# Kernel optimization log

Hardware: AMD Instinct MI355X
Metric: run time of the kernel (lower is better)

The kernel has to match this reference:

```python
import jax, jax.numpy as jnp
import numpy as np
from jax import lax

NUM_HEADS = 8

def _conv2d(x, w, b, padding, rhs_dilation=(1, 1)):
    # x: NCHW, w: OIHW
    out = lax.conv_general_dilated(x, w, (1, 1), padding,
                                   rhs_dilation=rhs_dilation,
                                   dimension_numbers=('NCHW', 'OIHW', 'NCHW'))
    return out + b[None, :, None, None]

def _bn(x, scale, bias):
    # eval-mode batchnorm folded into per-channel affine
    return x * scale[None, :, None, None] + bias[None, :, None, None]

def setup_inputs() -> dict:
    key = jax.random.key(0)
    ks = jax.random.split(key, 12)
    B, C, H, W = 16, 256, 64, 64
    D = C // 2          # down_dim = 128
    Dq = D // 16        # weight bottleneck = 8
    return {
        'x':          jax.random.normal(ks[0], (B, C, H, W), jnp.float32),
        'conv2_w':    jax.random.normal(ks[1], (D, C, 3, 3), jnp.float32) * 0.02,
        'conv2_b':    jnp.zeros((D,), jnp.float32),
        'bn2_scale':  jax.random.uniform(ks[2], (D,), jnp.float32, 0.5, 1.5),
        'bn2_bias':   jax.random.normal(ks[3], (D,), jnp.float32) * 0.1,
        'temperature': jnp.ones((NUM_HEADS, 1, 1), jnp.float32),
        'w1_w':       jax.random.normal(ks[4], (Dq, D, 1, 1), jnp.float32) * 0.05,
        'w1_b':       jnp.zeros((Dq,), jnp.float32),
        'bnw_scale':  jax.random.uniform(ks[5], (Dq,), jnp.float32, 0.5, 1.5),
        'bnw_bias':   jax.random.normal(ks[6], (Dq,), jnp.float32) * 0.1,
        'w2_w':       jax.random.normal(ks[7], (D, Dq, 1, 1), jnp.float32) * 0.05,
        'w2_b':       jnp.zeros((D,), jnp.float32),
    }

def _l2_normalize_complex(z, eps=1e-12):
    # torch F.normalize on complex: divide by L2 norm of |z| along last dim
    n = jnp.sqrt(jnp.sum(jnp.real(z * jnp.conj(z)), axis=-1, keepdims=True))
    return z / jnp.maximum(n, eps)

def reference(x, conv2_w, conv2_b, bn2_scale, bn2_bias, temperature,
              w1_w, w1_b, bnw_scale, bnw_bias, w2_w, w2_b):
    # conv2 branch: 3x3 conv with dilation=3, padding=3 -> BN -> ReLU
    conv2 = jax.nn.relu(_bn(_conv2d(x, conv2_w, conv2_b,
                                    ((3, 3), (3, 3)), rhs_dilation=(3, 3)),
                            bn2_scale, bn2_bias))
    b, c, h, w = conv2.shape
    f = jnp.fft.fft2(conv2)                      # complex64, (b,c,h,w); q=k=v=tepqkv
    cp = c // NUM_HEADS
    qkv = f.reshape(b, NUM_HEADS, cp, h * w)     # 'b (head c) h w -> b head c (h w)'
    qn = _l2_normalize_complex(qkv)
    kn = qn
    # complex attention logits, temperature broadcast over heads
    attn = jnp.einsum('bhin,bhjn->bhij', qn, kn) * temperature.astype(attn_dtype := qn.dtype)
    # dual real/imag softmax reassembled into complex
    attn = lax.complex(jax.nn.softmax(attn.real, axis=-1),
                       jax.nn.softmax(attn.imag, axis=-1))
    out_f = jnp.einsum('bhij,bhjn->bhin', attn, qkv)
    # torch.fft.ifft2 default dims=(-2,-1): here over (c, h*w) axes — faithful
    out_f = jnp.abs(jnp.fft.ifft2(out_f)).reshape(b, c, h, w)
    # gating branch on real part of spectrum
    g = jax.nn.relu(_bn(_conv2d(f.real, w1_w, w1_b, ((0, 0), (0, 0))),
                        bnw_scale, bnw_bias))
    g = jax.nn.sigmoid(_conv2d(g, w2_w, w2_b, ((0, 0), (0, 0))))
    out_l = jnp.abs(jnp.fft.ifft2(g * f))        # ifft2 over (h, w)
    out = jnp.concatenate([out_f, out_l], axis=1)
    return out + x
```

## Files before the change

kernel.cpp:

```cpp
#include <hip/hip_runtime.h>

typedef unsigned short u16;
typedef short short8 __attribute__((ext_vector_type(8)));
typedef float f32x4 __attribute__((ext_vector_type(4)));

#define MF(a,b,c) __builtin_amdgcn_mfma_f32_16x16x32_bf16(a,b,c,0,0,0)

__device__ __forceinline__ float bu2f(u16 u){
  return __uint_as_float(((unsigned int)u) << 16);
}
__device__ __forceinline__ u16 f2bu(float f){
  unsigned int b = __float_as_uint(f);
  unsigned int r = (b + 0x7FFFu + ((b >> 16) & 1u)) >> 16;
  return (u16)r;
}
__device__ __forceinline__ void ld4a(float* d, const float* p){
  float4 v = *(const float4*)p;
  d[0]=v.x; d[1]=v.y; d[2]=v.z; d[3]=v.w;
}
__device__ __forceinline__ void st4(float* p, const float* s){
  *(float4*)p = make_float4(s[0], s[1], s[2], s[3]);
}
__device__ __forceinline__ void ld4b(float* d, const u16* p){
  ushort4 v = *(const ushort4*)p;
  d[0]=bu2f(v.x); d[1]=bu2f(v.y); d[2]=bu2f(v.z); d[3]=bu2f(v.w);
}
__device__ __forceinline__ void st4b(u16* p, const float* s){
  ushort4 v;
  v.x=f2bu(s[0]); v.y=f2bu(s[1]); v.z=f2bu(s[2]); v.w=f2bu(s[3]);
  *(ushort4*)p = v;
}
__device__ __forceinline__ ushort4 pk4(f32x4 v){
  ushort4 u; u.x=f2bu(v[0]); u.y=f2bu(v[1]); u.z=f2bu(v[2]); u.w=f2bu(v[3]); return u;
}
__device__ __forceinline__ short8 mulpk(short8 g, short8 f){
  short8 o;
  #pragma unroll
  for (int e = 0; e < 8; ++e)
    o[e] = (short)f2bu(bu2f((u16)g[e])*bu2f((u16)f[e]));
  return o;
}

#define TABF_RE   0
#define TABF_IM   4096
#define TABIF_RE  8192
#define TABIF_IM  12288
#define TABTW_RE  16384
#define TABTW_IM  20480
#define NORMS_OFF 24576
#define MMAT_OFF  26624
#define FLAG_OFF  92160
#define PRM_OFF   92224
#define WT_OFF    94848
#define DFT16_OFF 242304
#define F32_END   389760
#define P_CB   0
#define P_BNS  128
#define P_BNB  256
#define P_TEMP 384
#define P_W1   400
#define P_B1   1424
#define P_S1   1432
#define P_BB1  1440
#define P_W2   1456
#define P_B2   2480
#define BPLANE    8388608

__global__ void k_detect(const u16* __restrict__ xv, int* __restrict__ flag){
  const int t = threadIdx.x;
  int huge = 0;
  for (int i = 0; i < 16; ++i){
    u16 u = xv[(t*16 + i)*2];
    int e = (u >> 7) & 0xFF;
    huge += (e >= 0xC0) ? 1 : 0;
  }
  #pragma unroll
  for (int off = 32; off > 0; off >>= 1) huge += __shfl_down(huge, off, 64);
  if (t == 0) flag[0] = (huge >= 8) ? 1 : 0;
}

__global__ void k_tables(float* ws){
  int idx = blockIdx.x*256 + threadIdx.x;
  int j = idx >> 6, k = idx & 63;
  int jk = j*k;
  float s, c;
  sincospif(-(float)(jk & 63)/32.0f, &s, &c);
  ws[TABF_RE+idx] = c; ws[TABF_IM+idx] = s;
  sincospif((float)(jk & 63)/32.0f, &s, &c);
  ws[TABIF_RE+idx] = c*(1.f/64.f); ws[TABIF_IM+idx] = s*(1.f/64.f);
  sincospif((float)jk/2048.0f, &s, &c);
  ws[TABTW_RE+idx] = c; ws[TABTW_IM+idx] = s;
}

__global__ void k_dftprep(u16* __restrict__ m){
  int idx = blockIdx.x*256 + threadIdx.x;
  int j = idx >> 6, k = idx & 63;
  int jk = (j*k) & 63;
  float s, c;
  sincospif(-(float)jk/32.0f, &s, &c);
  m[idx]        = f2bu(c);
  m[4096+idx]   = f2bu(s);
  sincospif((float)jk/32.0f, &s, &c);
  m[8192+idx]   = f2bu(c*(1.f/64.f));
  m[12288+idx]  = f2bu(s*(1.f/64.f));
}

__global__ void k_pack(const void* cb, const void* bns, const void* bnb, const void* temp,
                       const void* w1, const void* b1, const void* s1, const void* bb1,
                       const void* w2, const void* b2,
                       const int* __restrict__ flg, float* __restrict__ P){
  const int t = threadIdx.x;
  const int f32 = *flg;
  if (f32){
    for (int i = t; i < 128; i += 256){
      P[P_CB+i]  = ((const float*)cb)[i];
      P[P_BNS+i] = ((const float*)bns)[i];
      P[P_BNB+i] = ((const float*)bnb)[i];
      P[P_B2+i]  = ((const float*)b2)[i];
    }
    for (int i = t; i < 1024; i += 256){
      P[P_W1+i] = ((const float*)w1)[i];
      P[P_W2+i] = ((const float*)w2)[i];
    }
    if (t < 8){
      P[P_TEMP+t] = ((const float*)temp)[t];
      P[P_B1+t]   = ((const float*)b1)[t];
      P[P_S1+t]   = ((const float*)s1)[t];
      P[P_BB1+t]  = ((const float*)bb1)[t];
    }
  } else {
    for (int i = t; i < 128; i += 256){
      P[P_CB+i]  = bu2f(((const u16*)cb)[i]);
      P[P_BNS+i] = bu2f(((const u16*)bns)[i]);
      P[P_BNB+i] = bu2f(((const u16*)bnb)[i]);
      P[P_B2+i]  = bu2f(((const u16*)b2)[i]);
    }
    for (int i = t; i < 1024; i += 256){
      P[P_W1+i] = bu2f(((const u16*)w1)[i]);
      P[P_W2+i] = bu2f(((const u16*)w2)[i]);
    }
    if (t < 8){
      P[P_TEMP+t] = bu2f(((const u16*)temp)[t]);
      P[P_B1+t]   = bu2f(((const u16*)b1)[t]);
      P[P_S1+t]   = bu2f(((const u16*)s1)[t]);
      P[P_BB1+t]  = bu2f(((const u16*)bb1)[t]);
    }
  }
}

__global__ void k_wprep2(const void* __restrict__ w, u16* __restrict__ wT2,
                         const float* __restrict__ prm, const int* __restrict__ flg){
  const int f32 = *flg;
  int U = blockIdx.x*256 + threadIdx.x;
  if (U < 294912){
    int j = U & 7;
    int E = U >> 3;
    int n = E & 127;
    int o = (E >> 7) & 3;
    int tc = E >> 9;
    int chunk = tc & 7, tap = tc >> 3;
    int c = chunk*32 + o*8 + j;
    int src = n*2304 + c*9 + tap;
    float v = f32 ? ((const float*)w)[src] : bu2f(((const u16*)w)[src]);
    wT2[U] = f2bu(v * prm[P_BNS + n]);
  }
}

__global__ __launch_bounds__(256) void k_trans(const void* __restrict__ x, u16* __restrict__ xt,
                                               const int* __restrict__ flg){
  __shared__ u16 L[256*66];
  const int t = threadIdx.x;
  const int b = blockIdx.x >> 6, h = blockIdx.x & 63;
  const int f32m = __builtin_amdgcn_readfirstlane(*flg);
  if (f32m){
    const float* xf = (const float*)x;
    for (int i = t; i < 16384; i += 256){
      int c = i >> 6, w = i & 63;
      L[c*66 + w] = f2bu(xf[((b*256 + c)*64 + h)*64 + w]);
    }
  } else {
    const u16* xb = (const u16*)x;
    for (int i = t; i < 16384; i += 256){
      int c = i >> 6, w = i & 63;
      L[c*66 + w] = xb[((b*256 + c)*64 + h)*64 + w];
    }
  }
  __syncthreads();
  u16* dst = xt + ((b*64 + h)*64)*256;
  for (int j = t; j < 16384; j += 256){
    int w = j >> 8, c = j & 255;
    dst[w*256 + c] = L[c*66 + w];
  }
}

__global__ __launch_bounds__(512) void k_cmm(const u16* __restrict__ xt, const u16* __restrict__ wT2,
                                             const float* __restrict__ prm, u16* __restrict__ A){
  __shared__ __align__(16) uint4 smW4[8192];
  const int t = threadIdx.x;
  const int bb = blockIdx.x >> 4;
  const int mtile = blockIdx.x & 15;
  const int h0 = mtile*4;
  const int lane = t & 63, wave = t >> 6;
  const int wrow = wave >> 1, wcol = wave & 1;
  const int quad = lane >> 4, lr = lane & 15;

  f32x4 acc[4][4];
  #pragma unroll
  for (int mi = 0; mi < 4; ++mi)
    #pragma unroll
    for (int j = 0; j < 4; ++j)
      acc[mi][j] = (f32x4){0.f,0.f,0.f,0.f};

  const short8 zz = {0,0,0,0,0,0,0,0};

  {
    const uint4* src = (const uint4*)wT2;
    uint4 stg[8];
    #pragma unroll
    for (int i = 0; i < 8; ++i) stg[i] = src[t + 512*i];
    #pragma unroll
    for (int i = 0; i < 8; ++i) smW4[t + 512*i] = stg[i];
  }
  __syncthreads();

  for (int tap = 0; tap < 9; ++tap){
    const int buf = tap & 1;
    const int ky = tap/3, kx = tap - ky*3;

    uint4 stg[8];
    if (tap < 8){
      const uint4* src = (const uint4*)(wT2 + (tap+1)*32768);
      #pragma unroll
      for (int i = 0; i < 8; ++i) stg[i] = src[t + 512*i];
    }

    const u16* smB = (const u16*)(smW4 + buf*4096);
    const int hg = h0 + wrow + 3*ky - 3;
    const bool hok = ((unsigned)hg < 64u);
    const u16* abase = xt + ((bb*64 + hg)*64)*256 + quad*8;

    for (int chunk = 0; chunk < 8; ++chunk){
      short8 av[4];
      #pragma unroll
      for (int mi = 0; mi < 4; ++mi){
        const int wg = mi*16 + lr + 3*kx - 3;
        short8 v = zz;
        if (hok && ((unsigned)wg < 64u))
          v = *(const short8*)(abase + wg*256 + chunk*32);
        av[mi] = v;
      }
      short8 bv[4];
      #pragma unroll
      for (int j = 0; j < 4; ++j)
        bv[j] = *(const short8*)(smB + (chunk*512 + quad*128 + (wcol*4+j)*16 + lr)*8);
      #pragma unroll
      for (int mi = 0; mi < 4; ++mi)
        #pragma unroll
        for (int j = 0; j < 4; ++j)
          acc[mi][j] = MF(av[mi], bv[j], acc[mi][j]);
    }

    if (tap < 8){
      uint4* dst = smW4 + (buf^1)*4096;
      #pragma unroll
      for (int i = 0; i < 8; ++i) dst[t + 512*i] = stg[i];
    }
    __syncthreads();
  }

  float* C = (float*)smW4;
  u16* outb = A + (bb*128)*4096 + mtile*256;
  const int ch32 = wcol*16 + lr;
  for (int nt2 = 0; nt2 < 4; ++nt2){
    #pragma unroll
    for (int mi = 0; mi < 4; ++mi)
      #pragma unroll
      for (int r = 0; r < 4; ++r){
        const int m = wrow*64 + mi*16 + quad*4 + r;
        C[ch32*261 + m] = acc[mi][nt2][r];
      }
    __syncthreads();
    #pragma unroll
    for (int dd = 0; dd < 16; ++dd){
      const int idx = dd*512 + t;
      const int c32 = idx >> 8, m = idx & 255;
      const int d = (c32 >> 4)*64 + nt2*16 + (c32 & 15);
      const float bi = prm[P_CB + d]*prm[P_BNS + d] + prm[P_BNB + d];
      const float v = fmaxf(C[c32*261 + m] + bi, 0.f);
      outb[d*4096 + m] = f2bu(v);
    }
    __syncthreads();
  }
}

__global__ __launch_bounds__(256) void k_fft2_m(const u16* __restrict__ A, u16* __restrict__ Frb,
                                                u16* __restrict__ Fib, const u16* __restrict__ dft){
  __shared__ __align__(16) u16 TTr[64*72], TTi[64*72];
  const int bc = blockIdx.x, t = threadIdx.x;
  const int lane = t & 63, wave = t >> 6;
  const int quad = lane >> 4, lr = lane & 15;
  const u16* EFr = dft;
  const u16* EFi = dft + 4096;
  const u16* img = A + bc*4096;
  #pragma unroll
  for (int mi = 0; mi < 4; ++mi){
    f32x4 ar = {0.f,0.f,0.f,0.f}, ai = {0.f,0.f,0.f,0.f};
    #pragma unroll
    for (int ks = 0; ks < 2; ++ks){
      short8 av = *(const short8*)(img + (mi*16+lr)*64 + ks*32 + quad*8);
      short8 br = *(const short8*)(EFr + (wave*16+lr)*64 + ks*32 + quad*8);
      short8 bi = *(const short8*)(EFi + (wave*16+lr)*64 + ks*32 + quad*8);
      ar = MF(av, br, ar); ai = MF(av, bi, ai);
    }
    *(ushort4*)(TTr + (wave*16+lr)*72 + mi*16 + quad*4) = pk4(ar);
    *(ushort4*)(TTi + (wave*16+lr)*72 + mi*16 + quad*4) = pk4(ai);
  }
  __syncthreads();
  #pragma unroll
  for (int nt = 0; nt < 4; ++nt){
    f32x4 a1={0.f,0.f,0.f,0.f}, a2={0.f,0.f,0.f,0.f}, a3={0.f,0.f,0.f,0.f}, a4={0.f,0.f,0.f,0.f};
    #pragma unroll
    for (int ks = 0; ks < 2; ++ks){
      short8 tr = *(const short8*)(TTr + (wave*16+lr)*72 + ks*32 + quad*8);
      short8 ti = *(const short8*)(TTi + (wave*16+lr)*72 + ks*32 + quad*8);
      short8 br = *(const short8*)(EFr + (nt*16+lr)*64 + ks*32 + quad*8);
      short8 bi = *(const short8*)(EFi + (nt*16+lr)*64 + ks*32 + quad*8);
      a1 = MF(tr, br, a1); a2 = MF(ti, bi, a2);
      a3 = MF(tr, bi, a3); a4 = MF(ti, br, a4);
    }
    f32x4 fr, fi;
    #pragma unroll
    for (int r = 0; r < 4; ++r){ fr[r] = a1[r]-a2[r]; fi[r] = a3[r]+a4[r]; }
    const int flat = (nt*16+lr)*64 + wave*16 + quad*4;
    *(ushort4*)(Frb + bc*4096 + flat) = pk4(fr);
    *(ushort4*)(Fib + bc*4096 + flat) = pk4(fi);
  }
}

__global__ __launch_bounds__(256) void k_attn1(const u16* __restrict__ Frb,
                                               const u16* __restrict__ Fib,
                                               float* __restrict__ part){
  __shared__ float R[4][4][256];
  const int blk = blockIdx.x;
  const int bh = blk >> 4, chunk = blk & 15;
  const int t = threadIdx.x, lane = t & 63, wave = t >> 6;
  const int quad = lane >> 4, lr = lane & 15;
  const u16* fr = Frb + bh*65536;
  const u16* fi = Fib + bh*65536;
  const int c0 = chunk*256 + wave*64;
  f32x4 a1={0.f,0.f,0.f,0.f}, a2={0.f,0.f,0.f,0.f}, a3={0.f,0.f,0.f,0.f}, a4={0.f,0.f,0.f,0.f};
  #pragma unroll
  for (int ks = 0; ks < 2; ++ks){
    const int off = lr*4096 + c0 + ks*32 + quad*8;
    short8 ar = *(const short8*)(fr + off);
    short8 ai = *(const short8*)(fi + off);
    a1 = MF(ar, ar, a1); a2 = MF(ai, ai, a2);
    a3 = MF(ar, ai, a3); a4 = MF(ai, ar, a4);
  }
  #pragma unroll
  for (int r = 0; r < 4; ++r){
    const int mn = (quad*4 + r)*16 + lr;
    R[wave][0][mn] = a1[r];
    R[wave][1][mn] = a2[r];
    R[wave][2][mn] = a3[r];
    R[wave][3][mn] = a4[r];
  }
  __syncthreads();
  float* dst = part + blk*1024;
  #pragma unroll
  for (int q = 0; q < 4; ++q)
    dst[q*256 + t] = R[0][q][t] + R[1][q][t] + R[2][q][t] + R[3][q][t];
}

__global__ __launch_bounds__(256) void k_attn2(const float* __restrict__ part,
                                               const float* __restrict__ prm,
                                               float* __restrict__ wsM){
  __shared__ float AR[16][17], AI[16][17], NR[16];
  const int bh = blockIdx.x;
  const int h = bh & 7;
  const int t = threadIdx.x;
  const float* p = part + bh*16384;
  float s1=0.f, s2=0.f, s3=0.f, s4=0.f;
  #pragma unroll
  for (int ch = 0; ch < 16; ++ch){
    s1 += p[ch*1024 +       t];
    s2 += p[ch*1024 + 256 + t];
    s3 += p[ch*1024 + 512 + t];
    s4 += p[ch*1024 + 768 + t];
  }
  const int m = t >> 4, n = t & 15;
  if (m == n) NR[m] = fmaxf(sqrtf(fmaxf(s1 + s2, 0.f)), 1e-12f);
  __syncthreads();
  const float sc = prm[P_TEMP + h] / (NR[m]*NR[n]);
  AR[m][n] = (s1 - s2)*sc;
  AI[m][n] = (s3 + s4)*sc;
  __syncthreads();
  if (t < 32){
    float* row = (t < 16) ? AR[t & 15] : AI[t & 15];
    float mx = row[0];
    for (int j2 = 1; j2 < 16; ++j2) mx = fmaxf(mx, row[j2]);
    float s = 0.f, e[16];
    for (int j2 = 0; j2 < 16; ++j2){ e[j2] = expf(row[j2] - mx); s += e[j2]; }
    float inv = 1.f/s;
    for (int j2 = 0; j2 < 16; ++j2) row[j2] = e[j2]*inv;
  }
  __syncthreads();
  {
    const int mi = t >> 4, mj = t & 15;
    float mr = 0.f, mim = 0.f;
    #pragma unroll
    for (int pp = 0; pp < 16; ++pp){
      float sv, cv;
      sincospif((float)((mi*pp) & 15)/8.0f, &sv, &cv);
      const float arv = AR[pp][mj], aiv = AI[pp][mj];
      mr  += cv*arv - sv*aiv;
      mim += cv*aiv + sv*arv;
    }
    wsM[bh*512 + t*2]     = mr*(1.f/16.f);
    wsM[bh*512 + t*2 + 1] = mim*(1.f/16.f);
  }
}

__global__ __launch_bounds__(256) void k_gate(const u16* __restrict__ Frb,
                                              const float* __restrict__ prm,
                                              u16* __restrict__ g){
  __shared__ float W1T[128][8];
  __shared__ float W2[128][8];
  __shared__ float B1v[8], S1v[8], BB1v[8];
  __shared__ float B2v[128];
  const int t = threadIdx.x;
  for (int i = t; i < 1024; i += 256){
    W1T[i & 127][i >> 7] = prm[P_W1 + i];
    W2[i >> 3][i & 7]    = prm[P_W2 + i];
  }
  if (t < 8){ B1v[t] = prm[P_B1+t]; S1v[t] = prm[P_S1+t]; BB1v[t] = prm[P_BB1+t]; }
  if (t < 128) B2v[t] = prm[P_B2+t];
  __syncthreads();
  const int pix = blockIdx.x*256 + t;
  const int b = pix >> 12, n = pix & 4095;
  const u16* fr = Frb + b*128*4096 + n;
  float q[8] = {};
  for (int c = 0; c < 128; ++c){
    const float v = bu2f(fr[c*4096]);
    float wa[4], wb[4];
    ld4a(wa, &W1T[c][0]); ld4a(wb, &W1T[c][4]);
    #pragma unroll
    for (int k = 0; k < 4; ++k){ q[k] = fmaf(wa[k], v, q[k]); q[4+k] = fmaf(wb[k], v, q[4+k]); }
  }
  float qa[8];
  #pragma unroll
  for (int k = 0; k < 8; ++k)
    qa[k] = fmaxf(fmaf(q[k] + B1v[k], S1v[k], BB1v[k]), 0.f);
  u16* grow = g + b*128*4096 + n;
  for (int c = 0; c < 128; ++c){
    float wa[4], wb[4];
    ld4a(wa, &W2[c][0]); ld4a(wb, &W2[c][4]);
    float acc = B2v[c];
    #pragma unroll
    for (int k = 0; k < 4; ++k) acc += wa[k]*qa[k] + wb[k]*qa[4+k];
    grow[c*4096] = f2bu(1.f/(1.f + expf(-acc)));
  }
}

__global__ __launch_bounds__(256) void k_outl_m(const u16* __restrict__ Frb, const u16* __restrict__ Fib,
                                                const u16* __restrict__ g, const void* __restrict__ x,
                                                float* __restrict__ out, const u16* __restrict__ dft,
                                                const int* __restrict__ flg){
  __shared__ __align__(16) u16 TTr[64*72], TTi[64*72];
  const int bc = blockIdx.x, t = threadIdx.x;
  const int b = bc >> 7, c = bc & 127;
  const int lane = t & 63, wave = t >> 6;
  const int quad = lane >> 4, lr = lane & 15;
  const int f32m = __builtin_amdgcn_readfirstlane(*flg);
  const u16* EIr = dft + 8192;
  const u16* EIi = dft + 12288;
  const u16* pg = g   + bc*4096;
  const u16* pr = Frb + bc*4096;
  const u16* pi = Fib + bc*4096;
  #pragma unroll
  for (int mi = 0; mi < 4; ++mi){
    f32x4 a1={0.f,0.f,0.f,0.f}, a2={0.f,0.f,0.f,0.f}, a3={0.f,0.f,0.f,0.f}, a4={0.f,0.f,0.f,0.f};
    #pragma unroll
    for (int ks = 0; ks < 2; ++ks){
      const int ao = (mi*16+lr)*64 + ks*32 + quad*8;
      short8 gv = *(const short8*)(pg + ao);
      short8 apr = mulpk(gv, *(const short8*)(pr + ao));
      short8 api = mulpk(gv, *(const short8*)(pi + ao));
      const int bo = (wave*16+lr)*64 + ks*32 + quad*8;
      short8 br = *(const short8*)(EIr + bo);
      short8 bi = *(const short8*)(EIi + bo);
      a1 = MF(apr, br, a1); a2 = MF(api, bi, a2);
      a3 = MF(apr, bi, a3); a4 = MF(api, br, a4);
    }
    f32x4 tr, ti;
    #pragma unroll
    for (int r = 0; r < 4; ++r){ tr[r] = a1[r]-a2[r]; ti[r] = a3[r]+a4[r]; }
    *(ushort4*)(TTr + (wave*16+lr)*72 + mi*16 + quad*4) = pk4(tr);
    *(ushort4*)(TTi + (wave*16+lr)*72 + mi*16 + quad*4) = pk4(ti);
  }
  __syncthreads();
  #pragma unroll
  for (int nt = 0; nt < 4; ++nt){
    f32x4 a1={0.f,0.f,0.f,0.f}, a2={0.f,0.f,0.f,0.f}, a3={0.f,0.f,0.f,0.f}, a4={0.f,0.f,0.f,0.f};
    #pragma unroll
    for (int ks = 0; ks < 2; ++ks){
      short8 tr = *(const short8*)(TTr + (wave*16+lr)*72 + ks*32 + quad*8);
      short8 ti = *(const short8*)(TTi + (wave*16+lr)*72 + ks*32 + quad*8);
      const int bo = (nt*16+lr)*64 + ks*32 + quad*8;
      short8 br = *(const short8*)(EIr + bo);
      short8 bi = *(const short8*)(EIi + bo);
      a1 = MF(tr, br, a1); a2 = MF(ti, bi, a2);
      a3 = MF(tr, bi, a3); a4 = MF(ti, br, a4);
    }
    const int o = (b*256 + 128 + c)*4096 + (nt*16+lr)*64 + wave*16 + quad*4;
    float xr[4];
    if (f32m) ld4a(xr, (const float*)x + o); else ld4b(xr, (const u16*)x + o);
    float ov[4];
    #pragma unroll
    for (int r = 0; r < 4; ++r){
      float yr = a1[r]-a2[r], yi = a3[r]+a4[r];
      ov[r] = sqrtf(yr*yr + yi*yi) + xr[r];
    }
    st4(out + o, ov);
  }
}

__global__ __launch_bounds__(256) void k_ifft4096_m(u16* __restrict__ Frb, u16* __restrict__ Fib,
                                                    const float* __restrict__ ws,
                                                    const u16* __restrict__ dft){
  __shared__ __align__(16) u16 A2Tr[64*72], A2Ti[64*72], Cr[64*72], Ci[64*72];
  const int bc = blockIdx.x, t = threadIdx.x;
  const int lane = t & 63, wave = t >> 6;
  const int quad = lane >> 4, lr = lane & 15;
  const u16* EIr = dft + 8192;
  const u16* EIi = dft + 12288;
  const float* twr = ws + TABTW_RE;
  const float* twi = ws + TABTW_IM;
  u16* fr = Frb + bc*4096;
  u16* fi = Fib + bc*4096;
  for (int i = t; i < 4096; i += 256){
    int n1 = i >> 6, n2 = i & 63;
    A2Tr[n2*72 + n1] = fr[i];
    A2Ti[n2*72 + n1] = fi[i];
  }
  __syncthreads();
  #pragma unroll
  for (int nt = 0; nt < 4; ++nt){
    f32x4 a1={0.f,0.f,0.f,0.f}, a2={0.f,0.f,0.f,0.f}, a3={0.f,0.f,0.f,0.f}, a4={0.f,0.f,0.f,0.f};
    #pragma unroll
    for (int ks = 0; ks < 2; ++ks){
      const int ao = (wave*16+lr)*64 + ks*32 + quad*8;
      short8 Ar = *(const short8*)(EIr + ao);
      short8 Ai = *(const short8*)(EIi + ao);
      short8 br = *(const short8*)(A2Tr + (nt*16+lr)*72 + ks*32 + quad*8);
      short8 bi = *(const short8*)(A2Ti + (nt*16+lr)*72 + ks*32 + quad*8);
      a1 = MF(Ar, br, a1); a2 = MF(Ai, bi, a2);
      a3 = MF(Ar, bi, a3); a4 = MF(Ai, br, a4);
    }
    #pragma unroll
    for (int r = 0; r < 4; ++r){
      const int k1 = wave*16 + quad*4 + r;
      const int n2 = nt*16 + lr;
      const float trv = a1[r]-a2[r], tiv = a3[r]+a4[r];
      const float wr = twr[k1*64 + n2], wi = twi[k1*64 + n2];
      Cr[k1*72 + n2] = f2bu(trv*wr - tiv*wi);
      Ci[k1*72 + n2] = f2bu(trv*wi + tiv*wr);
    }
  }
  __syncthreads();
  #pragma unroll
  for (int nt = 0; nt < 4; ++nt){
    f32x4 a1={0.f,0.f,0.f,0.f}, a2={0.f,0.f,0.f,0.f}, a3={0.f,0.f,0.f,0.f}, a4={0.f,0.f,0.f,0.f};
    #pragma unroll
    for (int ks = 0; ks < 2; ++ks){
      short8 Ar = *(const short8*)(Cr + (wave*16+lr)*72 + ks*32 + quad*8);
      short8 Ai = *(const short8*)(Ci + (wave*16+lr)*72 + ks*32 + quad*8);
      const int bo = (nt*16+lr)*64 + ks*32 + quad*8;
      short8 br = *(const short8*)(EIr + bo);
      short8 bi = *(const short8*)(EIi + bo);
      a1 = MF(Ar, br, a1); a2 = MF(Ai, bi, a2);
      a3 = MF(Ar, bi, a3); a4 = MF(Ai, br, a4);
    }
    f32x4 zr, zi;
    #pragma unroll
    for (int r = 0; r < 4; ++r){ zr[r] = a1[r]-a2[r]; zi[r] = a3[r]+a4[r]; }
    const int flat = (nt*16+lr)*64 + wave*16 + quad*4;
    *(ushort4*)(fr + flat) = pk4(zr);
    *(ushort4*)(fi + flat) = pk4(zi);
  }
}

__global__ __launch_bounds__(256) void k_outf(const u16* __restrict__ Zr, const u16* __restrict__ Zi,
                                              const float* __restrict__ wsM, const void* __restrict__ x,
                                              float* __restrict__ out, const int* __restrict__ flg){
  __shared__ float MreT[16][20], MimT[16][20];
  const int gb = blockIdx.x;
  const int bh = gb & 127, nch = gb >> 7;
  const int b = bh >> 3, h = bh & 7;
  const int t = threadIdx.x;
  const int f32m = __builtin_amdgcn_readfirstlane(*flg);
  {
    const int i = t >> 4, j = t & 15;
    MreT[j][i] = wsM[bh*512 + t*2];
    MimT[j][i] = wsM[bh*512 + t*2 + 1];
  }
  __syncthreads();
  const int i0 = (t & 3)*4;
  const int nn = nch*256 + (t >> 2)*4;
  const u16* zr = Zr + (b*128 + h*16)*4096 + nn;
  const u16* zi = Zi + (b*128 + h*16)*4096 + nn;
  float accr[4][4] = {}, acci[4][4] = {};
  #pragma unroll
  for (int j = 0; j < 16; ++j){
    float mr[4], mi[4], vr[4], vi[4];
    ld4a(mr, &MreT[j][i0]);
    ld4a(mi, &MimT[j][i0]);
    ld4b(vr, zr + j*4096);
    ld4b(vi, zi + j*4096);
    #pragma unroll
    for (int i = 0; i < 4; ++i)
      #pragma unroll
      for (int n = 0; n < 4; ++n){
        accr[i][n] += mr[i]*vr[n] - mi[i]*vi[n];
        acci[i][n] += mr[i]*vi[n] + mi[i]*vr[n];
      }
  }
  #pragma unroll
  for (int i = 0; i < 4; ++i){
    const int o = (b*256 + h*16 + i0 + i)*4096 + nn;
    float xr[4];
    if (f32m) ld4a(xr, (const float*)x + o); else ld4b(xr, (const u16*)x + o);
    float ov[4];
    #pragma unroll
    for (int n = 0; n < 4; ++n)
      ov[n] = sqrtf(accr[i][n]*accr[i][n] + acci[i][n]*acci[i][n]) + xr[n];
    st4(out + o, ov);
  }
}

extern "C" void kernel_launch(void* const* d_in, const int* in_sizes, int n_in,
                              void* d_out, int out_size, void* d_ws, size_t ws_size,
                              hipStream_t stream) {
  const void* x        = d_in[0];
  const void* conv2_w  = d_in[1];
  const void* conv2_b  = d_in[2];
  const void* bn2_s    = d_in[3];
  const void* bn2_b    = d_in[4];
  const void* temp     = d_in[5];
  const void* w1_w     = d_in[6];
  const void* w1_b     = d_in[7];
  const void* bnw_s    = d_in[8];
  const void* bnw_b    = d_in[9];
  const void* w2_w     = d_in[10];
  const void* w2_b     = d_in[11];
  float* out = (float*)d_out;
  float* wsf = (float*)d_ws;

  if (ws_size < (size_t)(F32_END*4) + 3u*(size_t)BPLANE*2u) return;

  int* flag = (int*)(wsf + FLAG_OFF);
  float* prm = wsf + PRM_OFF;
  u16* wT2 = (u16*)(wsf + WT_OFF);
  u16* dft = (u16*)(wsf + DFT16_OFF);
  u16* wsb = (u16*)(wsf + F32_END);
  u16* Frb = wsb;
  u16* Fib = wsb + BPLANE;
  u16* xt  = wsb;
  u16* Ab  = wsb + 2*BPLANE;
  u16* g   = Ab;
  float* part = (float*)Ab;

  k_detect<<<1, 64, 0, stream>>>((const u16*)x, flag);
  k_tables<<<16, 256, 0, stream>>>(wsf);
  k_dftprep<<<16, 256, 0, stream>>>(dft);
  k_pack<<<1, 256, 0, stream>>>(conv2_b, bn2_s, bn2_b, temp, w1_w, w1_b, bnw_s, bnw_b,
                                w2_w, w2_b, flag, prm);
  k_wprep2<<<1152, 256, 0, stream>>>(conv2_w, wT2, prm, flag);
  k_trans<<<1024, 256, 0, stream>>>(x, xt, flag);
  k_cmm<<<256, 512, 0, stream>>>(xt, wT2, prm, Ab);
  k_fft2_m<<<2048, 256, 0, stream>>>(Ab, Frb, Fib, dft);
  k_attn1<<<2048, 256, 0, stream>>>(Frb, Fib, part);
  k_attn2<<<128, 256, 0, stream>>>(part, prm, wsf + MMAT_OFF);
  k_gate<<<256, 256, 0, stream>>>(Frb, prm, g);
  k_outl_m<<<2048, 256, 0, stream>>>(Frb, Fib, g, x, out, dft, flag);
  k_ifft4096_m<<<2048, 256, 0, stream>>>(Frb, Fib, wsf, dft);
  k_outf<<<2048, 256, 0, stream>>>(Frb, Fib, wsf + MMAT_OFF, x, out, flag);
}
```

Baseline: 482.7 us.

## Single-buffer conv weights in LDS to fit two blocks per CU, remap block order

The conv implicit-GEMM kernel drops double-buffered weight staging and halves its LDS footprint to 64KB, loading each tap's weights synchronously between barriers. It adds launch_bounds minimum of 2 blocks so two blocks can co-reside per CU. Block index is remapped so consecutive blocks span different batches for the same row tile, changing L2 locality. The cost is that the prefetch/compute overlap within a block is lost, and it relies on the second resident block to hide it. Register pressure is also constrained by the new bound.

```diff
diff --git a/kernel.cpp b/kernel.cpp
--- a/kernel.cpp
+++ b/kernel.cpp
@@ -193,12 +193,13 @@
   }
 }
 
-__global__ __launch_bounds__(512) void k_cmm(const u16* __restrict__ xt, const u16* __restrict__ wT2,
-                                             const float* __restrict__ prm, u16* __restrict__ A){
-  __shared__ __align__(16) uint4 smW4[8192];
+__global__ __launch_bounds__(512, 2) void k_cmm(const u16* __restrict__ xt, const u16* __restrict__ wT2,
+                                                const float* __restrict__ prm, u16* __restrict__ A){
+  __shared__ __align__(16) uint4 sm4[4096];
   const int t = threadIdx.x;
-  const int bb = blockIdx.x >> 4;
-  const int mtile = blockIdx.x & 15;
+  const int blk = blockIdx.x;
+  const int bb = (blk & 7) + 8*(blk >> 7);
+  const int mtile = (blk >> 3) & 15;
   const int h0 = mtile*4;
   const int lane = t & 63, wave = t >> 6;
   const int wrow = wave >> 1, wcol = wave & 1;
@@ -211,30 +212,19 @@
     for (int j = 0; j < 4; ++j)
       acc[mi][j] = (f32x4){0.f,0.f,0.f,0.f};
 
+  const u16* smB = (const u16*)sm4;
   const short8 zz = {0,0,0,0,0,0,0,0};
 
-  {
-    const uint4* src = (const uint4*)wT2;
-    uint4 stg[8];
-    #pragma unroll
-    for (int i = 0; i < 8; ++i) stg[i] = src[t + 512*i];
-    #pragma unroll
-    for (int i = 0; i < 8; ++i) smW4[t + 512*i] = stg[i];
-  }
-  __syncthreads();
-
   for (int tap = 0; tap < 9; ++tap){
-    const int buf = tap & 1;
     const int ky = tap/3, kx = tap - ky*3;
-
-    uint4 stg[8];
-    if (tap < 8){
-      const uint4* src = (const uint4*)(wT2 + (tap+1)*32768);
+    __syncthreads();
+    {
+      const uint4* src = (const uint4*)(wT2 + tap*32768);
       #pragma unroll
-      for (int i = 0; i < 8; ++i) stg[i] = src[t + 512*i];
-    }
-
-    const u16* smB = (const u16*)(smW4 + buf*4096);
+      for (int i = 0; i < 8; ++i) sm4[t + 512*i] = src[t + 512*i];
+    }
+    __syncthreads();
+
     const int hg = h0 + wrow + 3*ky - 3;
     const bool hok = ((unsigned)hg < 64u);
     const u16* abase = xt + ((bb*64 + hg)*64)*256 + quad*8;
@@ -259,18 +249,12 @@
         for (int j = 0; j < 4; ++j)
           acc[mi][j] = MF(av[mi], bv[j], acc[mi][j]);
     }
-
-    if (tap < 8){
-      uint4* dst = smW4 + (buf^1)*4096;
-      #pragma unroll
-      for (int i = 0; i < 8; ++i) dst[t + 512*i] = stg[i];
-    }
-    __syncthreads();
-  }
-
-  float* C = (float*)smW4;
+  }
+
+  float* C = (float*)sm4;
   u16* outb = A + (bb*128)*4096 + mtile*256;
   const int ch32 = wcol*16 + lr;
+  __syncthreads();
   for (int nt2 = 0; nt2 < 4; ++nt2){
     #pragma unroll
     for (int mi = 0; mi < 4; ++mi)
```

Result: faster. 449.3 us (-6.9%).
